# Performance work log

Measured on AMD Instinct MI355X. Metric: run time of the kernel, lower is better.

## Reference

```python
import jax, jax.numpy as jnp
import numpy as np

KROT = 8        # number of pairwise-rotation layers (hard-coded in Rotation)
GROUP = 128     # rotation group size (hard-coded)
QGS = 128       # quantization group size (hard-coded in RotateLinearAWQMarlinInt4)


def setup_inputs() -> dict:
    rng = np.random.default_rng(0)
    M, K, N = 32, 8192, 28672
    G = K // QGS  # 64 quant groups
    shifts = np.arange(8, dtype=np.uint32) * 4
    # activations
    x = jnp.asarray(rng.standard_normal((M, K)), dtype=jnp.float16)
    # int4 weights packed 8-per-int32 along the out dim (nibble j of word n -> column n*8+j)
    nib = rng.integers(0, 16, size=(K, N // 8, 8), dtype=np.uint32)
    qweight = jnp.asarray((nib << shifts).sum(-1, dtype=np.uint32).view(np.int32))  # (K, N//8)
    znib = rng.integers(0, 16, size=(G, N // 8, 8), dtype=np.uint32)
    qzeros = jnp.asarray((znib << shifts).sum(-1, dtype=np.uint32).view(np.int32))  # (G, N//8)
    scales = jnp.asarray(rng.uniform(0.001, 0.01, (G, N)), dtype=jnp.float16)
    bias = jnp.asarray(rng.standard_normal(N) * 0.01, dtype=jnp.float16)
    # rotation params: per-layer angles over all K//2 pairs; one local permutation of
    # 0..127 per layer, shared across all K//GROUP groups (as in Rotation.__init__)
    theta = jnp.asarray(rng.uniform(-0.2, 0.2, (KROT, K // 2)), dtype=jnp.float16)
    pairs = jnp.asarray(np.stack([rng.permutation(GROUP) for _ in range(KROT)]).astype(np.int32))  # (KROT, 128)
    channel_scales = jnp.asarray(rng.uniform(0.5, 2.0, (1, K)), dtype=jnp.float16)
    return dict(x=x, qweight=qweight, qzeros=qzeros, scales=scales, bias=bias,
                theta=theta, pairs=pairs, channel_scales=channel_scales)


def _rotate(x, pairs, theta, channel_scales):
    # x: (M, K). Apply KROT layers of Givens rotations on channel pairs within each
    # 128-wide group, then per-channel scaling.
    M, K = x.shape
    ng = K // GROUP
    xg = x.reshape(M, ng, GROUP)
    for k in range(KROT):
        p = pairs[k]                      # (128,) local permutation
        i, j = p[0::2], p[1::2]           # (64,) disjoint index sets
        th = theta[k].reshape(ng, GROUP // 2).astype(jnp.float32)  # (ng, 64) per-group angles
        c = jnp.cos(th).astype(x.dtype)
        s = jnp.sin(th).astype(x.dtype)
        xi = xg[:, :, i]
        xj = xg[:, :, j]
        xg = xg.at[:, :, i].set(c * xi - s * xj)
        xg = xg.at[:, :, j].set(s * xi + c * xj)
    return xg.reshape(M, K) * channel_scales


def _dequant(qweight, qzeros, scales):
    # unpack 8 uint4 nibbles per int32 along the out dim; dequant per quant group
    K = qweight.shape[0]
    shifts = jnp.arange(8, dtype=jnp.int32) * 4
    w = ((qweight[:, :, None] >> shifts) & 0xF).reshape(K, -1)       # (K, N) ints 0..15
    z = ((qzeros[:, :, None] >> shifts) & 0xF).reshape(qzeros.shape[0], -1)  # (G, N)
    zf = jnp.repeat(z.astype(scales.dtype), QGS, axis=0)             # (K, N)
    sf = jnp.repeat(scales, QGS, axis=0)                             # (K, N)
    return (w.astype(scales.dtype) - zf) * sf


def reference(x, qweight, qzeros, scales, bias, theta, pairs, channel_scales):
    xr = _rotate(x, pairs, theta, channel_scales)   # (M, K)
    W = _dequant(qweight, qzeros, scales)           # (K, N)
    return xr @ W + bias
```

## Files before the change

kernel.cpp:

```cpp
#include <hip/hip_runtime.h>
#include <hip/hip_bf16.h>

using uint32   = unsigned int;
using ushort_t = unsigned short;
using short8   = __attribute__((ext_vector_type(8))) short;
using uint4v   = __attribute__((ext_vector_type(4))) uint32;
using floatx16 = __attribute__((ext_vector_type(16))) float;

#define M_DIM 32
#define K_DIM 8192
#define N_DIM 28672
#define QROW  (N_DIM/8)
#define KSPLIT 8
#define BN    256
#define CH    128
#define NCH   8
#define TSTRIDE 132

typedef __attribute__((address_space(3))) uint32 lds_u32;
typedef const __attribute__((address_space(1))) uint32 glb_u32;

__device__ ushort_t g_xr2[M_DIM * K_DIM];
__device__ float    g_S[64 * M_DIM];

__device__ __forceinline__ float bf2f(ushort_t u){
  unsigned int v = ((unsigned int)u) << 16;
  return __builtin_bit_cast(float, v);
}
__device__ __forceinline__ ushort_t f2bf(float f){
  return __builtin_bit_cast(ushort_t, __float2bfloat16(f));
}

__global__ __launch_bounds__(256) void rotate_kernel(
    const float* __restrict__ x, const float* __restrict__ theta,
    const int* __restrict__ pairs, const float* __restrict__ cs)
{
  __shared__ float xb[4][128];
  const int u    = threadIdx.x >> 6;
  const int lane = threadIdx.x & 63;
  const int id   = blockIdx.x * 4 + u;
  const int m    = id >> 6;
  const int g    = id & 63;
  const float* xp = x + m*K_DIM + g*128;
  int   ip[8], jp[8];
  float cv[8], sv[8];
  #pragma unroll
  for (int k = 0; k < 8; ++k){
    ip[k] = pairs[k*128 + 2*lane];
    jp[k] = pairs[k*128 + 2*lane + 1];
    const float th = theta[k*(K_DIM/2) + g*64 + lane];
    cv[k] = cosf(th); sv[k] = sinf(th);
  }
  xb[u][lane]    = xp[lane];
  xb[u][lane+64] = xp[lane+64];
  #pragma unroll
  for (int k = 0; k < 8; ++k){
    __syncthreads();
    const float xi = xb[u][ip[k]], xj = xb[u][jp[k]];
    xb[u][ip[k]] = cv[k]*xi - sv[k]*xj;
    xb[u][jp[k]] = sv[k]*xi + cv[k]*xj;
  }
  __syncthreads();
  const int base = g*128;
  const int k0 = base + lane, k1 = base + lane + 64;
  const ushort_t b0 = f2bf(xb[u][lane]    * cs[k0]);
  const ushort_t b1 = f2bf(xb[u][lane+64] * cs[k1]);
  g_xr2[(((size_t)(k0>>3))*32 + m)*8 + (k0&7)] = b0;
  g_xr2[(((size_t)(k1>>3))*32 + m)*8 + (k1&7)] = b1;
  float sum = bf2f(b0) + bf2f(b1);
  #pragma unroll
  for (int d = 32; d > 0; d >>= 1) sum += __shfl_xor(sum, d, 64);
  if (lane == 0) g_S[g*M_DIM + m] = sum;
}

__global__ __launch_bounds__(256) void init2_kernel(
    const uint32* __restrict__ qz, const float* __restrict__ scales,
    const float* __restrict__ bias, float* __restrict__ out)
{
  const int n = blockIdx.x*256 + threadIdx.x;
  const uint32 sh = (uint32)((n & 7)*4);
  float acc[M_DIM];
  const float b = bias[n];
  #pragma unroll
  for (int m = 0; m < M_DIM; ++m) acc[m] = b;
  #pragma unroll 1
  for (int g = 0; g < 64; ++g){
    const float s  = scales[(size_t)g*N_DIM + n];
    const uint32 zq = qz[(size_t)g*QROW + (n>>3)];
    const float t  = s * (float)(128u + ((zq >> sh) & 15u));
    #pragma unroll
    for (int m = 0; m < M_DIM; ++m)
      acc[m] = fmaf(-t, g_S[g*M_DIM + m], acc[m]);
  }
  #pragma unroll
  for (int m = 0; m < M_DIM; ++m) out[(size_t)m*N_DIM + n] = acc[m];
}

__global__ __launch_bounds__(512, 4) void gemm_kernel(
    const uint32* __restrict__ qw, const float* __restrict__ scales,
    float* __restrict__ out)
{
  __shared__ uint32   T[32*TSTRIDE];
  __shared__ ushort_t A[2][CH*32];
  const int bid  = blockIdx.x;
  const int ks   = bid & 7;
  const int nb   = bid >> 3;
  const int tid  = threadIdx.x;
  const int w    = tid >> 6;
  const int lane = tid & 63;
  const int l31  = lane & 31;
  const int koct = lane >> 5;
  const int n0   = nb * BN;
  const int n    = n0 + w*32 + l31;
  const uint32 sh = (uint32)((l31 & 7)*4);
  const int col  = w*4 + (l31 >> 3);
  const int k0   = ks * (NCH*CH);

  const int brow = tid >> 3;
  const int bcq  = tid & 7;
  const uint32* bbase = qw + (size_t)(k0 + brow)*QROW + (n0>>3) + bcq*4;
  const ushort_t* abase = g_xr2 + (size_t)k0*32;

  float accT[16];
  #pragma unroll
  for (int r = 0; r < 16; ++r) accT[r] = 0.f;

  uint4v bv[2][2];

  auto stageA = [&](int c){
    const ushort_t* gp = abase + (size_t)c*CH*32 + w*512 + lane*8;
    ushort_t* lp = &A[c & 1][0] + w*512;
    __builtin_amdgcn_global_load_lds((glb_u32*)gp, (lds_u32*)lp, 16, 0, 0);
  };

  bv[0][0] = *(const uint4v*)(bbase);
  bv[0][1] = *(const uint4v*)(bbase + (size_t)64*QROW);
  stageA(0);
  #pragma unroll
  for (int j = 0; j < 4; ++j){
    T[(bcq*4 + j)*TSTRIDE + brow]      = bv[0][0][j];
    T[(bcq*4 + j)*TSTRIDE + brow + 64] = bv[0][1][j];
  }

  #pragma unroll
  for (int c = 0; c < NCH; ++c){
    __syncthreads();
    const int cb = c & 1, nx = cb ^ 1;
    if (c + 1 < NCH){
      const uint32* bb = bbase + (size_t)(c+1)*CH*QROW;
      bv[nx][0] = *(const uint4v*)(bb);
      bv[nx][1] = *(const uint4v*)(bb + (size_t)64*QROW);
      stageA(c+1);
    }
    const float s = scales[(size_t)(ks*NCH + c)*N_DIM + n];
    floatx16 acc;
    #pragma unroll
    for (int r = 0; r < 16; ++r) acc[r] = 0.f;
    #pragma unroll
    for (int kk = 0; kk < 8; ++kk){
      const short8 a = *(const short8*)(&A[cb][((kk*2 + koct)*32 + l31)*8]);
      const uint32* tp = &T[col*TSTRIDE + kk*16 + koct*8];
      const uint4v p0 = *(const uint4v*)(tp);
      const uint4v p1 = *(const uint4v*)(tp + 4);
      uint4v bp;
      bp.x = ((p0.x >> sh) & 15u) | (((p0.y >> sh) & 15u) << 16) | 0x43004300u;
      bp.y = ((p0.z >> sh) & 15u) | (((p0.w >> sh) & 15u) << 16) | 0x43004300u;
      bp.z = ((p1.x >> sh) & 15u) | (((p1.y >> sh) & 15u) << 16) | 0x43004300u;
      bp.w = ((p1.z >> sh) & 15u) | (((p1.w >> sh) & 15u) << 16) | 0x43004300u;
      acc = __builtin_amdgcn_mfma_f32_32x32x16_bf16(
                a, __builtin_bit_cast(short8, bp), acc, 0, 0, 0);
    }
    #pragma unroll
    for (int r = 0; r < 16; ++r) accT[r] = fmaf(s, acc[r], accT[r]);
    __syncthreads();
    if (c + 1 < NCH){
      #pragma unroll
      for (int j = 0; j < 4; ++j){
        T[(bcq*4 + j)*TSTRIDE + brow]      = bv[nx][0][j];
        T[(bcq*4 + j)*TSTRIDE + brow + 64] = bv[nx][1][j];
      }
    }
  }
  #pragma unroll
  for (int r = 0; r < 16; ++r){
    const int row = (r & 3) + 8*(r >> 2) + 4*koct;
    atomicAdd(out + (size_t)row*N_DIM + n, accT[r]);
  }
}

extern "C" void kernel_launch(void* const* d_in, const int* in_sizes, int n_in,
                              void* d_out, int out_size, void* d_ws, size_t ws_size,
                              hipStream_t stream)
{
  const float*  x      = (const float*)d_in[0];
  const uint32* qw     = (const uint32*)d_in[1];
  const uint32* qz     = (const uint32*)d_in[2];
  const float*  scales = (const float*)d_in[3];
  const float*  bias   = (const float*)d_in[4];
  const float*  theta  = (const float*)d_in[5];
  const int*    pairs  = (const int*)d_in[6];
  const float*  cs     = (const float*)d_in[7];
  float* out = (float*)d_out;

  rotate_kernel<<<dim3((M_DIM*64)/4), dim3(256), 0, stream>>>(x, theta, pairs, cs);
  init2_kernel<<<dim3(N_DIM/256), dim3(256), 0, stream>>>(qz, scales, bias, out);
  gemm_kernel<<<dim3((N_DIM/BN)*KSPLIT), dim3(512), 0, stream>>>(qw, scales, out);
}
```

Before: 248.6 us.

## Fuse zero-point correction into GEMM and use per-wave private LDS tiles without barriers

Moves the zero-point/offset correction (t * S) out of the separate init kernel into the GEMM epilogue of each chunk, leaving a trivial bias-fill kernel. It also gives each wave its own transposed weight tile in LDS and drops the block-wide __syncthreads, and reads the activation operand straight from global memory instead of staging it in LDS. The goal is to remove a long serial init kernel and cut block-wide barrier stalls. The cost is repeated global reads of the activations and qzeros per wave, and a larger LDS footprint that may lower occupancy.

New measurement: 255.8 us. 1.03x slower.

```diff
diff --git a/kernel.cpp b/kernel.cpp
--- a/kernel.cpp
+++ b/kernel.cpp
@@ -5,6 +5,7 @@
 using ushort_t = unsigned short;
 using short8   = __attribute__((ext_vector_type(8))) short;
 using uint4v   = __attribute__((ext_vector_type(4))) uint32;
+using float4v  = __attribute__((ext_vector_type(4))) float;
 using floatx16 = __attribute__((ext_vector_type(16))) float;
 
 #define M_DIM 32
@@ -16,9 +17,6 @@
 #define CH    128
 #define NCH   8
 #define TSTRIDE 132
-
-typedef __attribute__((address_space(3))) uint32 lds_u32;
-typedef const __attribute__((address_space(1))) uint32 glb_u32;
 
 __device__ ushort_t g_xr2[M_DIM * K_DIM];
 __device__ float    g_S[64 * M_DIM];
@@ -73,35 +71,21 @@
   if (lane == 0) g_S[g*M_DIM + m] = sum;
 }
 
-__global__ __launch_bounds__(256) void init2_kernel(
-    const uint32* __restrict__ qz, const float* __restrict__ scales,
+__global__ __launch_bounds__(256) void bias_kernel(
     const float* __restrict__ bias, float* __restrict__ out)
 {
-  const int n = blockIdx.x*256 + threadIdx.x;
-  const uint32 sh = (uint32)((n & 7)*4);
-  float acc[M_DIM];
+  const int n  = (blockIdx.x % (N_DIM/256))*256 + threadIdx.x;
+  const int m0 = (blockIdx.x / (N_DIM/256))*8;
   const float b = bias[n];
   #pragma unroll
-  for (int m = 0; m < M_DIM; ++m) acc[m] = b;
-  #pragma unroll 1
-  for (int g = 0; g < 64; ++g){
-    const float s  = scales[(size_t)g*N_DIM + n];
-    const uint32 zq = qz[(size_t)g*QROW + (n>>3)];
-    const float t  = s * (float)(128u + ((zq >> sh) & 15u));
-    #pragma unroll
-    for (int m = 0; m < M_DIM; ++m)
-      acc[m] = fmaf(-t, g_S[g*M_DIM + m], acc[m]);
-  }
-  #pragma unroll
-  for (int m = 0; m < M_DIM; ++m) out[(size_t)m*N_DIM + n] = acc[m];
+  for (int m = 0; m < 8; ++m) out[(size_t)(m0+m)*N_DIM + n] = b;
 }
 
 __global__ __launch_bounds__(512, 4) void gemm_kernel(
-    const uint32* __restrict__ qw, const float* __restrict__ scales,
-    float* __restrict__ out)
+    const uint32* __restrict__ qw, const uint32* __restrict__ qz,
+    const float* __restrict__ scales, float* __restrict__ out)
 {
-  __shared__ uint32   T[32*TSTRIDE];
-  __shared__ ushort_t A[2][CH*32];
+  __shared__ uint32 T[8 * 2 * 4 * TSTRIDE];
   const int bid  = blockIdx.x;
   const int ks   = bid & 7;
   const int nb   = bid >> 3;
@@ -113,72 +97,77 @@
   const int n0   = nb * BN;
   const int n    = n0 + w*32 + l31;
   const uint32 sh = (uint32)((l31 & 7)*4);
-  const int col  = w*4 + (l31 >> 3);
+  const int colr = l31 >> 3;
   const int k0   = ks * (NCH*CH);
 
-  const int brow = tid >> 3;
-  const int bcq  = tid & 7;
-  const uint32* bbase = qw + (size_t)(k0 + brow)*QROW + (n0>>3) + bcq*4;
+  uint32* Tw = &T[w * (2*4*TSTRIDE)];
+
+  const uint32* bbase = qw + (size_t)k0*QROW + (n0>>3) + w*4;
   const ushort_t* abase = g_xr2 + (size_t)k0*32;
 
   float accT[16];
   #pragma unroll
   for (int r = 0; r < 16; ++r) accT[r] = 0.f;
 
-  uint4v bv[2][2];
+  uint4v bva[2], bvb[2];
+  bva[0] = *(const uint4v*)(bbase + (size_t)lane*QROW);
+  bvb[0] = *(const uint4v*)(bbase + (size_t)(lane+64)*QROW);
 
-  auto stageA = [&](int c){
-    const ushort_t* gp = abase + (size_t)c*CH*32 + w*512 + lane*8;
-    ushort_t* lp = &A[c & 1][0] + w*512;
-    __builtin_amdgcn_global_load_lds((glb_u32*)gp, (lds_u32*)lp, 16, 0, 0);
-  };
-
-  bv[0][0] = *(const uint4v*)(bbase);
-  bv[0][1] = *(const uint4v*)(bbase + (size_t)64*QROW);
-  stageA(0);
-  #pragma unroll
-  for (int j = 0; j < 4; ++j){
-    T[(bcq*4 + j)*TSTRIDE + brow]      = bv[0][0][j];
-    T[(bcq*4 + j)*TSTRIDE + brow + 64] = bv[0][1][j];
-  }
-
-  #pragma unroll
+  #pragma unroll 2
   for (int c = 0; c < NCH; ++c){
-    __syncthreads();
     const int cb = c & 1, nx = cb ^ 1;
+    uint32* Tc = Tw + cb*(4*TSTRIDE);
+    #pragma unroll
+    for (int j = 0; j < 4; ++j){
+      Tc[j*TSTRIDE + lane]      = bva[cb][j];
+      Tc[j*TSTRIDE + lane + 64] = bvb[cb][j];
+    }
     if (c + 1 < NCH){
       const uint32* bb = bbase + (size_t)(c+1)*CH*QROW;
-      bv[nx][0] = *(const uint4v*)(bb);
-      bv[nx][1] = *(const uint4v*)(bb + (size_t)64*QROW);
-      stageA(c+1);
+      bva[nx] = *(const uint4v*)(bb + (size_t)lane*QROW);
+      bvb[nx] = *(const uint4v*)(bb + (size_t)(lane+64)*QROW);
     }
-    const float s = scales[(size_t)(ks*NCH + c)*N_DIM + n];
+    const float  s  = scales[(size_t)(ks*NCH + c)*N_DIM + n];
+    const uint32 zq = qz[(size_t)(ks*NCH + c)*QROW + (n>>3)];
+    const ushort_t* ab = abase + (size_t)c*CH*32;
+
     floatx16 acc;
     #pragma unroll
     for (int r = 0; r < 16; ++r) acc[r] = 0.f;
+
     #pragma unroll
-    for (int kk = 0; kk < 8; ++kk){
-      const short8 a = *(const short8*)(&A[cb][((kk*2 + koct)*32 + l31)*8]);
-      const uint32* tp = &T[col*TSTRIDE + kk*16 + koct*8];
-      const uint4v p0 = *(const uint4v*)(tp);
-      const uint4v p1 = *(const uint4v*)(tp + 4);
-      uint4v bp;
-      bp.x = ((p0.x >> sh) & 15u) | (((p0.y >> sh) & 15u) << 16) | 0x43004300u;
-      bp.y = ((p0.z >> sh) & 15u) | (((p0.w >> sh) & 15u) << 16) | 0x43004300u;
-      bp.z = ((p1.x >> sh) & 15u) | (((p1.y >> sh) & 15u) << 16) | 0x43004300u;
-      bp.w = ((p1.z >> sh) & 15u) | (((p1.w >> sh) & 15u) << 16) | 0x43004300u;
-      acc = __builtin_amdgcn_mfma_f32_32x32x16_bf16(
-                a, __builtin_bit_cast(short8, bp), acc, 0, 0, 0);
+    for (int kh = 0; kh < 2; ++kh){
+      short8 av[4];
+      #pragma unroll
+      for (int i = 0; i < 4; ++i){
+        const int kk = kh*4 + i;
+        av[i] = *(const short8*)(ab + ((kk*2 + koct)*32 + l31)*8);
+      }
+      #pragma unroll
+      for (int i = 0; i < 4; ++i){
+        const int kk = kh*4 + i;
+        const uint32* tp = Tc + colr*TSTRIDE + kk*16 + koct*8;
+        const uint4v p0 = *(const uint4v*)(tp);
+        const uint4v p1 = *(const uint4v*)(tp + 4);
+        uint4v bp;
+        bp.x = ((p0.x >> sh) & 15u) | (((p0.y >> sh) & 15u) << 16) | 0x43004300u;
+        bp.y = ((p0.z >> sh) & 15u) | (((p0.w >> sh) & 15u) << 16) | 0x43004300u;
+        bp.z = ((p1.x >> sh) & 15u) | (((p1.y >> sh) & 15u) << 16) | 0x43004300u;
+        bp.w = ((p1.z >> sh) & 15u) | (((p1.w >> sh) & 15u) << 16) | 0x43004300u;
+        acc = __builtin_amdgcn_mfma_f32_32x32x16_bf16(
+                  av[i], __builtin_bit_cast(short8, bp), acc, 0, 0, 0);
+      }
     }
+    const float t = s * (float)(128u + ((zq >> sh) & 15u));
+    const float* Sg = &g_S[(size_t)(ks*NCH + c)*M_DIM];
+    float4v Sv[4];
     #pragma unroll
-    for (int r = 0; r < 16; ++r) accT[r] = fmaf(s, acc[r], accT[r]);
-    __syncthreads();
-    if (c + 1 < NCH){
-      #pragma unroll
-      for (int j = 0; j < 4; ++j){
-        T[(bcq*4 + j)*TSTRIDE + brow]      = bv[nx][0][j];
-        T[(bcq*4 + j)*TSTRIDE + brow + 64] = bv[nx][1][j];
-      }
+    for (int q = 0; q < 4; ++q)
+      Sv[q] = *(const float4v*)(Sg + q*8 + 4*koct);
+    #pragma unroll
+    for (int r = 0; r < 16; ++r){
+      accT[r] = fmaf(s, acc[r], accT[r]);
+      accT[r] = fmaf(-t, Sv[r >> 2][r & 3], accT[r]);
     }
   }
   #pragma unroll
@@ -203,6 +192,6 @@
   float* out = (float*)d_out;
 
   rotate_kernel<<<dim3((M_DIM*64)/4), dim3(256), 0, stream>>>(x, theta, pairs, cs);
-  init2_kernel<<<dim3(N_DIM/256), dim3(256), 0, stream>>>(qz, scales, bias, out);
-  gemm_kernel<<<dim3((N_DIM/BN)*KSPLIT), dim3(512), 0, stream>>>(qw, scales, out);
+  bias_kernel<<<dim3((N_DIM/256)*4), dim3(256), 0, stream>>>(bias, out);
+  gemm_kernel<<<dim3((N_DIM/BN)*KSPLIT), dim3(512), 0, stream>>>(qw, qz, scales, out);
 }
```
